# Performance work log

Measured on AMD Instinct MI355X. Metric: run time of the kernel, lower is better.

## Reference

```python
import jax, jax.numpy as jnp
import numpy as np

N_NODES = 20000
N_EDGES = 320000
NUM_RELS = 16
IN_FEAT = 256
OUT_FEAT = 256


def setup_inputs() -> dict:
    key = jax.random.key(0)
    k_h, k_w, k_n, k_s, k_d, k_r = jax.random.split(key, 6)
    h = jax.random.normal(k_h, (N_NODES, IN_FEAT), dtype=jnp.float32)
    weight = jax.random.normal(k_w, (NUM_RELS, IN_FEAT, OUT_FEAT), dtype=jnp.float32)
    norm = jax.random.uniform(k_n, (N_EDGES, 1), dtype=jnp.float32)
    src = jax.random.randint(k_s, (N_EDGES,), 0, N_NODES, dtype=jnp.int32)
    dst = jax.random.randint(k_d, (N_EDGES,), 0, N_NODES, dtype=jnp.int32)
    rel_type = jax.random.randint(k_r, (N_EDGES,), 0, NUM_RELS, dtype=jnp.int32)
    return {"h": h, "weight": weight, "norm": norm, "src": src, "dst": dst, "rel_type": rel_type}


def reference(h, weight, norm, src, dst, rel_type):
    # Transform every node feature by every relation weight once ([R, N, O]),
    # instead of gathering a full [E, in, out] weight tensor per edge.
    transformed = jnp.einsum('ni,rio->rno', h, weight)
    # Per-edge message: h[src] @ W[rel] scaled by edge norm -> [E, O]
    msg = transformed[rel_type, src] * norm
    # Scatter-sum messages into destination nodes (DGL mailbox sum reduce).
    out = jax.ops.segment_sum(msg, dst, num_segments=h.shape[0])
    # bias=None, activation=None in this configuration, so apply_func is identity.
    return out
```

## Files before the change

### kernel.cpp

```cpp
#include <hip/hip_runtime.h>
#include <stdint.h>

#define N_NODES_C 20000
#define N_EDGES_C 320000
#define NUM_RELS_C 16
#define FEAT_C 256
#define CAP_LOG2 6
#define GEMM_BLOCKS 5024
#define WS_FAST_BYTES 186497152ULL

typedef __bf16 bf16_t;
typedef __bf16 bf16x8 __attribute__((ext_vector_type(8)));
typedef __bf16 bf16x4 __attribute__((ext_vector_type(4)));
typedef float f32x4 __attribute__((ext_vector_type(4)));

__device__ __forceinline__ void async_load16(const void* g, void* l) {
  __builtin_amdgcn_global_load_lds(
      (__attribute__((address_space(1))) void*)const_cast<void*>(g),
      (__attribute__((address_space(3))) void*)l, 16, 0, 0);
}

__global__ void prep_fast_kernel(const float* __restrict__ h, bf16_t* __restrict__ hB,
                                 const float* __restrict__ W, bf16_t* __restrict__ Wt,
                                 int* __restrict__ cnt) {
  int b = blockIdx.x;
  int t = threadIdx.x;
  if (b < 5000) {
    int i = (b * 256 + t) * 4;
    float4 v = *(const float4*)(h + i);
    bf16x4 o = { (bf16_t)v.x, (bf16_t)v.y, (bf16_t)v.z, (bf16_t)v.w };
    *(bf16x4*)(hB + i) = o;
  } else if (b < 5256) {
    __shared__ bf16_t lds[64][66];
    int b2 = b - 5000;
    int r  = b2 >> 4;
    int i0 = ((b2 >> 2) & 3) << 6;
    int o0 = (b2 & 3) << 6;
    int tx = t & 15;
    int ty = t >> 4;
#pragma unroll
    for (int pass = 0; pass < 4; ++pass) {
      int il = ty + pass * 16;
      float4 v = *(const float4*)(W + (r << 16) + ((i0 + il) << 8) + o0 + tx * 4);
      lds[tx * 4 + 0][il] = (bf16_t)v.x;
      lds[tx * 4 + 1][il] = (bf16_t)v.y;
      lds[tx * 4 + 2][il] = (bf16_t)v.z;
      lds[tx * 4 + 3][il] = (bf16_t)v.w;
    }
    __syncthreads();
#pragma unroll
    for (int pass = 0; pass < 4; ++pass) {
      int ol = ty + pass * 16;
      bf16x4 pk = { lds[ol][tx * 4 + 0], lds[ol][tx * 4 + 1],
                    lds[ol][tx * 4 + 2], lds[ol][tx * 4 + 3] };
      *(bf16x4*)(Wt + (r << 16) + ((o0 + ol) << 8) + i0 + tx * 4) = pk;
    }
  } else {
    int idx = (b - 5256) * 256 + t;
    if (idx < N_NODES_C) cnt[idx] = 0;
  }
}

__global__ void prep_kernel(const float* __restrict__ h, bf16_t* __restrict__ hB,
                            const float* __restrict__ W, bf16_t* __restrict__ Wt,
                            const int* __restrict__ dst, int* __restrict__ dcur) {
  int b = blockIdx.x;
  int t = threadIdx.x;
  if (b < 5000) {
    int i = (b * 256 + t) * 4;
    float4 v = *(const float4*)(h + i);
    bf16x4 o = { (bf16_t)v.x, (bf16_t)v.y, (bf16_t)v.z, (bf16_t)v.w };
    *(bf16x4*)(hB + i) = o;
  } else if (b < 9096) {
    int g = (b - 5000) * 256 + t;
    int i = g & 255;
    int o = (g >> 8) & 255;
    int r = g >> 16;
    Wt[(r << 16) + (o << 8) + i] = (bf16_t)W[(r << 16) + (i << 8) + o];
  } else {
    int e = (b - 9096) * 256 + t;
    if (e < N_EDGES_C) atomicAdd(&dcur[dst[e]], 1);
  }
}

__global__ void scan_dst_kernel(int* __restrict__ dcur, int* __restrict__ dstart) {
  __shared__ unsigned short cnt[20224];
  __shared__ int wsum[4];
  const int CH = 79;
  int t = threadIdx.x;
  int base = t * CH;
  int sum = 0;
  for (int i = 0; i < CH; ++i) {
    int idx = base + i;
    int c = (idx < N_NODES_C) ? dcur[idx] : 0;
    cnt[idx] = (unsigned short)c;
    sum += c;
  }
  int v = sum;
#pragma unroll
  for (int off = 1; off < 64; off <<= 1) {
    int u = __shfl_up(v, off);
    if ((t & 63) >= off) v += u;
  }
  if ((t & 63) == 63) wsum[t >> 6] = v;
  __syncthreads();
  int add = 0;
  for (int w = 0; w < (t >> 6); ++w) add += wsum[w];
  int run = v - sum + add;
  for (int i = 0; i < CH; ++i) {
    int idx = base + i;
    if (idx < N_NODES_C) {
      int c = cnt[idx];
      dstart[idx] = run;
      dcur[idx] = run;
      run += c;
    }
  }
  if (t == 0) dstart[N_NODES_C] = N_EDGES_C;
}

__global__ void bucket_dst_kernel(const int* __restrict__ dst, const int* __restrict__ src,
                                  const int* __restrict__ rel, const float* __restrict__ norm,
                                  int* __restrict__ dcur, int2* __restrict__ bkt) {
  int e = blockIdx.x * blockDim.x + threadIdx.x;
  if (e < N_EDGES_C) {
    int pos = atomicAdd(&dcur[dst[e]], 1);
    int2 pk;
    pk.x = src[e] | (rel[e] << 16);
    pk.y = __float_as_int(norm[e]);
    bkt[pos] = pk;
  }
}

__global__ __launch_bounds__(256) void gemm_bucket_kernel(
    const bf16_t* __restrict__ hB, const bf16_t* __restrict__ Wt,
    bf16_t* __restrict__ Tb,
    const int* __restrict__ dst, const int* __restrict__ src,
    const int* __restrict__ rel, const float* __restrict__ norm,
    int* __restrict__ cnt, int2* __restrict__ bkt) {
  int bx = blockIdx.x;
  int tid = threadIdx.x;

  if (bx >= GEMM_BLOCKS) {
    int e = (bx - GEMM_BLOCKS) * 256 + tid;
    if (e < N_EDGES_C) {
      int d = dst[e];
      int pos = (d << CAP_LOG2) + atomicAdd(&cnt[d], 1);
      int2 pk;
      pk.x = src[e] | (rel[e] << 16);
      pk.y = __float_as_int(norm[e]);
      bkt[pos] = pk;
    }
    return;
  }

  int sub = bx & 31;
  int m0 = (bx >> 5) << 7;
  int r  = sub >> 1;
  int n0 = (sub & 1) << 7;

  __shared__ bf16_t Asm[3 * 128 * 32];
  __shared__ bf16_t Bsm[3 * 128 * 32];

  int lrow = tid >> 2;
  int pch = tid & 3;
  int rA0 = lrow, rA1 = lrow + 64;
  int lc0 = pch ^ ((rA0 >> 1) & 3);
  int lc1 = pch ^ ((rA1 >> 1) & 3);
  int gr0 = m0 + rA0; if (gr0 > N_NODES_C - 1) gr0 = N_NODES_C - 1;
  int gr1 = m0 + rA1; if (gr1 > N_NODES_C - 1) gr1 = N_NODES_C - 1;
  const char* gA0 = (const char*)(hB + (size_t)gr0 * FEAT_C) + lc0 * 16;
  const char* gA1 = (const char*)(hB + (size_t)gr1 * FEAT_C) + lc1 * 16;
  const char* gB0 = (const char*)(Wt + ((size_t)r * 256 + n0 + rA0) * FEAT_C) + lc0 * 16;
  const char* gB1 = (const char*)(Wt + ((size_t)r * 256 + n0 + rA1) * FEAT_C) + lc1 * 16;

  int wave = tid >> 6;
  int lane = tid & 63;
  int lq = lane >> 4;
  int lr = lane & 15;
  int wm = (wave >> 1) * 64;
  int wn = (wave & 1) * 64;
  int pc8 = (lq ^ ((lr >> 1) & 3)) * 8;

  f32x4 acc[4][4] = {};

#define STAGE(buf, t)                                             \
  do {                                                            \
    int kb_ = (t) * 64;                                           \
    char* aB_ = (char*)Asm + (buf) * 8192 + wave * 1024;          \
    char* bB_ = (char*)Bsm + (buf) * 8192 + wave * 1024;          \
    async_load16(gA0 + kb_, aB_);                                 \
    async_load16(gA1 + kb_, aB_ + 4096);                          \
    async_load16(gB0 + kb_, bB_);                                 \
    async_load16(gB1 + kb_, bB_ + 4096);                          \
  } while (0)

  STAGE(0, 0);
  STAGE(1, 1);

#pragma unroll
  for (int kk = 0; kk < 8; ++kk) {
    if (kk < 7) asm volatile("s_waitcnt vmcnt(4)" ::: "memory");
    else        asm volatile("s_waitcnt vmcnt(0)" ::: "memory");
    __builtin_amdgcn_s_barrier();
    __builtin_amdgcn_sched_barrier(0);
    const bf16_t* Ac = Asm + (kk % 3) * 4096;
    const bf16_t* Bc = Bsm + (kk % 3) * 4096;
    bf16x8 af[4], bfr[4];
#pragma unroll
    for (int mt = 0; mt < 4; ++mt) {
      int row = wm + mt * 16 + lr;
      af[mt] = *(const bf16x8*)&Ac[row * 32 + pc8];
    }
#pragma unroll
    for (int nt2 = 0; nt2 < 4; ++nt2) {
      int row = wn + nt2 * 16 + lr;
      bfr[nt2] = *(const bf16x8*)&Bc[row * 32 + pc8];
    }
    if (kk < 6) STAGE((kk + 2) % 3, kk + 2);
#pragma unroll
    for (int mt = 0; mt < 4; ++mt)
#pragma unroll
      for (int nt2 = 0; nt2 < 4; ++nt2)
        acc[mt][nt2] = __builtin_amdgcn_mfma_f32_16x16x32_bf16(af[mt], bfr[nt2], acc[mt][nt2], 0, 0, 0);
  }
#undef STAGE

#pragma unroll
  for (int mt = 0; mt < 4; ++mt) {
#pragma unroll
    for (int a = 0; a < 2; ++a) {
      int rg0 = a * 2, rg1 = rg0 + 1;
      union { bf16x4 v; long long u; } q0, q1;
      q0.v = (bf16x4){ (bf16_t)acc[mt][0][rg0], (bf16_t)acc[mt][1][rg0],
                       (bf16_t)acc[mt][2][rg0], (bf16_t)acc[mt][3][rg0] };
      q1.v = (bf16x4){ (bf16_t)acc[mt][0][rg1], (bf16_t)acc[mt][1][rg1],
                       (bf16_t)acc[mt][2][rg1], (bf16_t)acc[mt][3][rg1] };
      int odd = lr & 1;
      long long send = odd ? q0.u : q1.u;
      long long got = __shfl_xor(send, 1);
      union { bf16x8 v; long long u[2]; } w;
      w.u[0] = odd ? got : q0.u;
      w.u[1] = odd ? q1.u : got;
      int rg = rg0 + odd;
      int row = m0 + wm + mt * 16 + lq * 4 + rg;
      if (row < N_NODES_C) {
        int pos = n0 + wn + ((lr >> 1) << 3);
        *(bf16x8*)(Tb + (((size_t)r * N_NODES_C + row) << 8) + pos) = w.v;
      }
    }
  }
}

template <int MODE>
__global__ __launch_bounds__(256) void aggregate_kernel(
    const bf16_t* __restrict__ Tb, const int* __restrict__ meta,
    const int2* __restrict__ bkt, float* __restrict__ out) {
  int tid = threadIdx.x;
  int d = blockIdx.x * 4 + (tid >> 6);
  int lane = tid & 63;
  int h = lane >> 5;
  int l5 = lane & 31;
  int p0, p1;
  if (MODE == 0) { p0 = meta[d]; p1 = meta[d + 1]; }
  else           { p0 = d << CAP_LOG2; p1 = p0 + meta[d]; }
  int boff = l5 << 4;
  float acc[8] = {};
  int p = p0 + h;
  for (; p + 14 < p1; p += 16) {
    int2 m[8];
#pragma unroll
    for (int q = 0; q < 8; ++q) m[q] = bkt[p + 2 * q];
    bf16x8 v[8];
#pragma unroll
    for (int q = 0; q < 8; ++q)
      v[q] = *(const bf16x8*)((const char*)(Tb + (((size_t)(m[q].x >> 16) * N_NODES_C + (m[q].x & 0xFFFF)) << 8)) + boff);
#pragma unroll
    for (int q = 0; q < 8; ++q) {
      float nq = __int_as_float(m[q].y);
#pragma unroll
      for (int j = 0; j < 8; ++j) acc[j] += (float)v[q][j] * nq;
    }
  }
  for (; p + 2 < p1; p += 4) {
    int2 m0 = bkt[p];
    int2 m1 = bkt[p + 2];
    bf16x8 v0 = *(const bf16x8*)((const char*)(Tb + (((size_t)(m0.x >> 16) * N_NODES_C + (m0.x & 0xFFFF)) << 8)) + boff);
    bf16x8 v1 = *(const bf16x8*)((const char*)(Tb + (((size_t)(m1.x >> 16) * N_NODES_C + (m1.x & 0xFFFF)) << 8)) + boff);
    float n0 = __int_as_float(m0.y);
    float n1 = __int_as_float(m1.y);
#pragma unroll
    for (int j = 0; j < 8; ++j) acc[j] += (float)v0[j] * n0 + (float)v1[j] * n1;
  }
  if (p < p1) {
    int2 m0 = bkt[p];
    bf16x8 v0 = *(const bf16x8*)((const char*)(Tb + (((size_t)(m0.x >> 16) * N_NODES_C + (m0.x & 0xFFFF)) << 8)) + boff);
    float n0 = __int_as_float(m0.y);
#pragma unroll
    for (int j = 0; j < 8; ++j) acc[j] += (float)v0[j] * n0;
  }
  float s[8];
#pragma unroll
  for (int j = 0; j < 8; ++j) {
    s[j] = acc[j];
    s[j] += __shfl_xor(s[j], 32);
  }
  if (h == 0) {
    int g64 = (l5 >> 3) << 6;
    int lr4 = (l5 << 1) & 15;
    float* o = out + (size_t)d * FEAT_C + g64 + lr4;
#pragma unroll
    for (int j = 0; j < 4; ++j) {
      float2 w = { s[j], s[j + 4] };
      *(float2*)(o + j * 16) = w;
    }
  }
}

extern "C" void kernel_launch(void* const* d_in, const int* in_sizes, int n_in,
                              void* d_out, int out_size, void* d_ws, size_t ws_size,
                              hipStream_t stream) {
  const float* h    = (const float*)d_in[0];
  const float* W    = (const float*)d_in[1];
  const float* norm = (const float*)d_in[2];
  const int*   src  = (const int*)d_in[3];
  const int*   dst  = (const int*)d_in[4];
  const int*   rel  = (const int*)d_in[5];
  float* out = (float*)d_out;

  char* ws = (char*)d_ws;
  bf16_t* hB   = (bf16_t*)ws;
  bf16_t* Wt   = (bf16_t*)(ws + 10240000);
  bf16_t* Tb   = (bf16_t*)(ws + 12337152);

  if (ws_size >= WS_FAST_BYTES) {
    int* cnt  = (int*)(ws + 176177152);
    int2* bkt = (int2*)(ws + 176257152);
    prep_fast_kernel<<<5335, 256, 0, stream>>>(h, hB, W, Wt, cnt);
    gemm_bucket_kernel<<<GEMM_BLOCKS + 1250, 256, 0, stream>>>(
        hB, Wt, Tb, dst, src, rel, norm, cnt, bkt);
    aggregate_kernel<1><<<5000, 256, 0, stream>>>(Tb, cnt, bkt, out);
  } else {
    int* dstart  = (int*)(ws + 176177152);
    int* dcur    = (int*)(ws + 176257168);
    int2* bkt    = (int2*)(ws + 176337168);
    hipMemsetAsync(dcur, 0, N_NODES_C * sizeof(int), stream);
    prep_kernel<<<10346, 256, 0, stream>>>(h, hB, W, Wt, dst, dcur);
    scan_dst_kernel<<<1, 256, 0, stream>>>(dcur, dstart);
    bucket_dst_kernel<<<1250, 256, 0, stream>>>(dst, src, rel, norm, dcur, bkt);
    gemm_bucket_kernel<<<GEMM_BLOCKS, 256, 0, stream>>>(
        hB, Wt, Tb, nullptr, nullptr, nullptr, nullptr, nullptr, nullptr);
    aggregate_kernel<0><<<5000, 256, 0, stream>>>(Tb, dstart, bkt, out);
  }
}
```

Measured before the change: 184.8 us.

## Load GEMM B operand directly into registers and schedule bucket blocks first

The weight (B) tiles in the fused GEMM are no longer staged through LDS. Each lane now loads its B fragments straight from global memory into double-buffered registers, one k-step ahead, and the per-stage async copy count and vmcnt wait drop to match. This halves LDS use and LDS traffic per block, which may allow more resident blocks, at the cost of more register pressure and uncoalesced-looking global loads that rely on L2 hits. The edge-bucketing blocks also move to the front of the grid so their atomics are dispatched before the GEMM tiles.

```diff
diff --git a/kernel.cpp b/kernel.cpp
--- a/kernel.cpp
+++ b/kernel.cpp
@@ -6,6 +6,7 @@
 #define NUM_RELS_C 16
 #define FEAT_C 256
 #define CAP_LOG2 6
+#define BUCKET_BLOCKS 1250
 #define GEMM_BLOCKS 5024
 #define WS_FAST_BYTES 186497152ULL
 
@@ -137,12 +138,12 @@
     bf16_t* __restrict__ Tb,
     const int* __restrict__ dst, const int* __restrict__ src,
     const int* __restrict__ rel, const float* __restrict__ norm,
-    int* __restrict__ cnt, int2* __restrict__ bkt) {
+    int* __restrict__ cnt, int2* __restrict__ bkt, int bucket_blocks) {
   int bx = blockIdx.x;
   int tid = threadIdx.x;
 
-  if (bx >= GEMM_BLOCKS) {
-    int e = (bx - GEMM_BLOCKS) * 256 + tid;
+  if (bx < bucket_blocks) {
+    int e = bx * 256 + tid;
     if (e < N_EDGES_C) {
       int d = dst[e];
       int pos = (d << CAP_LOG2) + atomicAdd(&cnt[d], 1);
@@ -153,6 +154,7 @@
     }
     return;
   }
+  bx -= bucket_blocks;
 
   int sub = bx & 31;
   int m0 = (bx >> 5) << 7;
@@ -160,7 +162,6 @@
   int n0 = (sub & 1) << 7;
 
   __shared__ bf16_t Asm[3 * 128 * 32];
-  __shared__ bf16_t Bsm[3 * 128 * 32];
 
   int lrow = tid >> 2;
   int pch = tid & 3;
@@ -171,8 +172,6 @@
   int gr1 = m0 + rA1; if (gr1 > N_NODES_C - 1) gr1 = N_NODES_C - 1;
   const char* gA0 = (const char*)(hB + (size_t)gr0 * FEAT_C) + lc0 * 16;
   const char* gA1 = (const char*)(hB + (size_t)gr1 * FEAT_C) + lc1 * 16;
-  const char* gB0 = (const char*)(Wt + ((size_t)r * 256 + n0 + rA0) * FEAT_C) + lc0 * 16;
-  const char* gB1 = (const char*)(Wt + ((size_t)r * 256 + n0 + rA1) * FEAT_C) + lc1 * 16;
 
   int wave = tid >> 6;
   int lane = tid & 63;
@@ -182,49 +181,56 @@
   int wn = (wave & 1) * 64;
   int pc8 = (lq ^ ((lr >> 1) & 3)) * 8;
 
+  const char* pB[4];
+#pragma unroll
+  for (int nt = 0; nt < 4; ++nt)
+    pB[nt] = (const char*)Wt + (((size_t)(r << 8) + n0 + wn + nt * 16 + lr) << 9) + (lq << 4);
+
   f32x4 acc[4][4] = {};
+  bf16x8 bfr[2][4];
 
 #define STAGE(buf, t)                                             \
   do {                                                            \
     int kb_ = (t) * 64;                                           \
     char* aB_ = (char*)Asm + (buf) * 8192 + wave * 1024;          \
-    char* bB_ = (char*)Bsm + (buf) * 8192 + wave * 1024;          \
     async_load16(gA0 + kb_, aB_);                                 \
     async_load16(gA1 + kb_, aB_ + 4096);                          \
-    async_load16(gB0 + kb_, bB_);                                 \
-    async_load16(gB1 + kb_, bB_ + 4096);                          \
+  } while (0)
+
+#define LOADB(j)                                                  \
+  do {                                                            \
+    _Pragma("unroll")                                             \
+    for (int nt = 0; nt < 4; ++nt)                                \
+      bfr[(j) & 1][nt] = *(const bf16x8*)(pB[nt] + (j) * 64);     \
   } while (0)
 
   STAGE(0, 0);
   STAGE(1, 1);
+  LOADB(0);
 
 #pragma unroll
   for (int kk = 0; kk < 8; ++kk) {
-    if (kk < 7) asm volatile("s_waitcnt vmcnt(4)" ::: "memory");
+    if (kk < 7) asm volatile("s_waitcnt vmcnt(2)" ::: "memory");
     else        asm volatile("s_waitcnt vmcnt(0)" ::: "memory");
     __builtin_amdgcn_s_barrier();
     __builtin_amdgcn_sched_barrier(0);
     const bf16_t* Ac = Asm + (kk % 3) * 4096;
-    const bf16_t* Bc = Bsm + (kk % 3) * 4096;
-    bf16x8 af[4], bfr[4];
+    bf16x8 af[4];
 #pragma unroll
     for (int mt = 0; mt < 4; ++mt) {
       int row = wm + mt * 16 + lr;
       af[mt] = *(const bf16x8*)&Ac[row * 32 + pc8];
     }
-#pragma unroll
-    for (int nt2 = 0; nt2 < 4; ++nt2) {
-      int row = wn + nt2 * 16 + lr;
-      bfr[nt2] = *(const bf16x8*)&Bc[row * 32 + pc8];
-    }
+    if (kk < 7) LOADB(kk + 1);
     if (kk < 6) STAGE((kk + 2) % 3, kk + 2);
 #pragma unroll
     for (int mt = 0; mt < 4; ++mt)
 #pragma unroll
       for (int nt2 = 0; nt2 < 4; ++nt2)
-        acc[mt][nt2] = __builtin_amdgcn_mfma_f32_16x16x32_bf16(af[mt], bfr[nt2], acc[mt][nt2], 0, 0, 0);
+        acc[mt][nt2] = __builtin_amdgcn_mfma_f32_16x16x32_bf16(af[mt], bfr[kk & 1][nt2], acc[mt][nt2], 0, 0, 0);
   }
 #undef STAGE
+#undef LOADB
 
 #pragma unroll
   for (int mt = 0; mt < 4; ++mt) {
@@ -337,8 +343,8 @@
     int* cnt  = (int*)(ws + 176177152);
     int2* bkt = (int2*)(ws + 176257152);
     prep_fast_kernel<<<5335, 256, 0, stream>>>(h, hB, W, Wt, cnt);
-    gemm_bucket_kernel<<<GEMM_BLOCKS + 1250, 256, 0, stream>>>(
-        hB, Wt, Tb, dst, src, rel, norm, cnt, bkt);
+    gemm_bucket_kernel<<<BUCKET_BLOCKS + GEMM_BLOCKS, 256, 0, stream>>>(
+        hB, Wt, Tb, dst, src, rel, norm, cnt, bkt, BUCKET_BLOCKS);
     aggregate_kernel<1><<<5000, 256, 0, stream>>>(Tb, cnt, bkt, out);
   } else {
     int* dstart  = (int*)(ws + 176177152);
@@ -349,7 +355,7 @@
     scan_dst_kernel<<<1, 256, 0, stream>>>(dcur, dstart);
     bucket_dst_kernel<<<1250, 256, 0, stream>>>(dst, src, rel, norm, dcur, bkt);
     gemm_bucket_kernel<<<GEMM_BLOCKS, 256, 0, stream>>>(
-        hB, Wt, Tb, nullptr, nullptr, nullptr, nullptr, nullptr, nullptr);
+        hB, Wt, Tb, nullptr, nullptr, nullptr, nullptr, nullptr, nullptr, 0);
     aggregate_kernel<0><<<5000, 256, 0, stream>>>(Tb, dstart, bkt, out);
   }
 }
```

Measured after the change: 217.6 us. 1.18x slower.
